# Kernel optimization log

Hardware: AMD Instinct MI355X
Metric: run time of the kernel (lower is better)

Reference implementation:

```python
import jax, jax.numpy as jnp
import numpy as np

FX, FY, CX, CY = 320.0, 320.0, 320.0, 240.0
N_MEAS, N_MP, N_KF = 2_000_000, 100_000, 2_000


def setup_inputs() -> dict:
    key = jax.random.key(0)
    k1, k2, k3, k4 = jax.random.split(key, 4)
    tMP = jax.random.normal(k1, (N_MP, 3), jnp.float32)
    # poses: near-identity with a +5 z-translation so projective depth stays away from 0
    tKF = jnp.eye(4, dtype=jnp.float32)[None] + 0.05 * jax.random.normal(k2, (N_KF, 4, 4), jnp.float32)
    tKF = tKF.at[:, 2, 3].add(5.0)
    idxMP = jnp.arange(N_MP, dtype=jnp.int32)
    idxKF = jnp.arange(N_KF, dtype=jnp.int32)
    mKF = jax.random.randint(k3, (N_MEAS,), 0, N_KF).astype(jnp.float32)
    mMP = jax.random.randint(k4, (N_MEAS,), 0, N_MP).astype(jnp.float32)
    measurements = jnp.stack([mKF, mMP], axis=1)  # [N, 2] float ids
    return {"measurements": measurements, "tMP": tMP, "tKF": tKF, "idxMP": idxMP, "idxKF": idxKF}


def reference(measurements, tMP, tKF, idxMP, idxKF):
    # ID -> row-index join. Original does an O(N*K)/O(N*M) broadcast equality via
    # torch.where; ids here are sorted unique, so a sorted join (searchsorted)
    # yields identical indices without materializing the N x M compare.
    iKF = jnp.searchsorted(idxKF, measurements[:, 0].astype(jnp.int32))
    iMP = jnp.searchsorted(idxMP, measurements[:, 1].astype(jnp.int32))
    # homogeneous map points: [M, 4]
    tMPhomo = jnp.concatenate([tMP, jnp.ones((tMP.shape[0], 1), tMP.dtype)], axis=1)
    # gather + batched 4x4 pose @ point: [N, 4]
    pts = jnp.einsum('nij,nj->ni', tKF[iKF], tMPhomo[iMP])
    # perspective divide + intrinsics scale
    ptx = pts[:, 0] / pts[:, 2] * FX + CX
    pty = pts[:, 1] / pts[:, 2] * FY + CY
    return jnp.stack([ptx, pty], axis=1)  # [N, 2]
```

## Files before the change

### kernel.cpp

```cpp
#include <hip/hip_runtime.h>
#include <hip/hip_bf16.h>

#define FXK 320.0f
#define FYK 320.0f
#define CXK 320.0f
#define CYK 240.0f

#define MAX_KF 2048

typedef float float4u __attribute__((ext_vector_type(4), aligned(4)));

__device__ __forceinline__ void unpack_mp(float4u q, bool sh,
                                          float& x, float& y, float& z) {
    x = sh ? q.y : q.x;
    y = sh ? q.z : q.y;
    z = sh ? q.w : q.z;
}

__device__ __forceinline__ float4 project2(const float4* __restrict__ sPose,
                                           int kfa, float xa, float ya, float za,
                                           int kfb, float xb, float yb, float zb) {
    const float4* Pa = sPose + kfa * 3;
    const float4* Pb = sPose + kfb * 3;
    float4 a0 = Pa[0], a1 = Pa[1], a2 = Pa[2];
    float4 b0 = Pb[0], b1 = Pb[1], b2 = Pb[2];
    float pxa = a0.x * xa + a0.y * ya + a0.z * za + a0.w;
    float pya = a1.x * xa + a1.y * ya + a1.z * za + a1.w;
    float pza = a2.x * xa + a2.y * ya + a2.z * za + a2.w;
    float pxb = b0.x * xb + b0.y * yb + b0.z * zb + b0.w;
    float pyb = b1.x * xb + b1.y * yb + b1.z * zb + b1.w;
    float pzb = b2.x * xb + b2.y * yb + b2.z * zb + b2.w;
    float ia = 1.0f / pza;
    float ib = 1.0f / pzb;
    float4 r;
    r.x = pxa * ia * FXK + CXK;
    r.y = pya * ia * FYK + CYK;
    r.z = pxb * ib * FXK + CXK;
    r.w = pyb * ib * FYK + CYK;
    return r;
}

__global__ __launch_bounds__(1024, 1) void proj_kernel(
    const float4* __restrict__ meas4,
    const float*  __restrict__ tMP,
    const float4* __restrict__ tKF4,
    float4*       __restrict__ out4,
    const float*  __restrict__ meas,
    float*        __restrict__ out,
    int n,
    int nKF,
    int nMPf)
{
    __shared__ float4 sPose[MAX_KF * 3];
    const int tid = threadIdx.x;
    const int nChunks = nKF * 3;
    for (int c = tid; c < nChunks; c += blockDim.x) {
        int pose = c / 3;
        int row  = c - pose * 3;
        sPose[c] = tKF4[pose * 4 + row];
    }
    __syncthreads();

    const int nPairs = n >> 1;
    const int bdim   = blockDim.x;
    const int tile   = bdim * 2;
    const int sweep  = gridDim.x * tile;
    const int last4  = nMPf - 4;

    for (int base = blockIdx.x * tile; base < nPairs; base += sweep) {
        int i0 = base + tid;
        int i1 = i0 + bdim;
        bool v0 = i0 < nPairs;
        bool v1 = i1 < nPairs;

        float4 m0 = meas4[v0 ? i0 : 0];
        float4 m1 = meas4[v1 ? i1 : 0];

        int kfA = (int)m0.x, mpA = (int)m0.y;
        int kfB = (int)m0.z, mpB = (int)m0.w;
        int kfC = (int)m1.x, mpC = (int)m1.y;
        int kfD = (int)m1.z, mpD = (int)m1.w;

        int oA = mpA * 3, oB = mpB * 3, oC = mpC * 3, oD = mpD * 3;
        int cA = oA > last4 ? last4 : oA;
        int cB = oB > last4 ? last4 : oB;
        int cC = oC > last4 ? last4 : oC;
        int cD = oD > last4 ? last4 : oD;
        float4u qA = *(const float4u*)(tMP + cA);
        float4u qB = *(const float4u*)(tMP + cB);
        float4u qC = *(const float4u*)(tMP + cC);
        float4u qD = *(const float4u*)(tMP + cD);

        float xA, yA, zA, xB, yB, zB, xC, yC, zC, xD, yD, zD;
        unpack_mp(qA, cA != oA, xA, yA, zA);
        unpack_mp(qB, cB != oB, xB, yB, zB);
        unpack_mp(qC, cC != oC, xC, yC, zC);
        unpack_mp(qD, cD != oD, xD, yD, zD);

        float4 r0 = project2(sPose, kfA, xA, yA, zA, kfB, xB, yB, zB);
        if (v0) out4[i0] = r0;
        float4 r1 = project2(sPose, kfC, xC, yC, zC, kfD, xD, yD, zD);
        if (v1) out4[i1] = r1;
    }

    if ((n & 1) && blockIdx.x == 0 && tid == 0) {
        int j = n - 1;
        int kf = (int)meas[2 * j + 0];
        int mp = (int)meas[2 * j + 1];
        float x = tMP[3 * mp + 0];
        float y = tMP[3 * mp + 1];
        float z = tMP[3 * mp + 2];
        const float4* P = sPose + kf * 3;
        float4 a0 = P[0], a1 = P[1], a2 = P[2];
        float px = a0.x * x + a0.y * y + a0.z * z + a0.w;
        float py = a1.x * x + a1.y * y + a1.z * z + a1.w;
        float pz = a2.x * x + a2.y * y + a2.z * z + a2.w;
        float inv = 1.0f / pz;
        out[2 * j + 0] = px * inv * FXK + CXK;
        out[2 * j + 1] = py * inv * FYK + CYK;
    }
}

extern "C" void kernel_launch(void* const* d_in, const int* in_sizes, int n_in,
                              void* d_out, int out_size, void* d_ws, size_t ws_size,
                              hipStream_t stream) {
    const float* meas = (const float*)d_in[0];
    const float* tMP  = (const float*)d_in[1];
    const float* tKF  = (const float*)d_in[2];

    int n    = in_sizes[0] / 2;
    int nMPf = in_sizes[1];
    int nKF  = in_sizes[2] / 16;
    if (nKF > MAX_KF) nKF = MAX_KF;

    int nPairs = n >> 1;
    int threads = 1024;
    int tile = threads * 2;
    int blocks = (nPairs + tile - 1) / tile;
    if (blocks > 256) blocks = 256;
    if (blocks < 1) blocks = 1;

    proj_kernel<<<blocks, threads, 0, stream>>>(
        (const float4*)meas, tMP, (const float4*)tKF,
        (float4*)d_out, meas, (float*)d_out, n, nKF, nMPf);
}
```

Measured before the change: 84.30 us.

## Repack map points to aligned float4, pad pose LDS stride, use nontemporal I/O

Adds a pre-pass kernel that copies the 3-float map points into a 16-byte aligned float4 workspace, so the main kernel gathers each point with one aligned load and no clamp or select logic. The shared pose table now uses a 13-float stride to spread LDS bank accesses for random keyframe lookups. Measurement loads and output stores become nontemporal to avoid polluting cache. The cost is an extra kernel launch and a copy of the map points into a 1.6MB workspace on every call, and the packed path only runs when the workspace is large enough.

After: 90.44 us. 1.07x slower.

```diff
diff --git a/kernel.cpp b/kernel.cpp
--- a/kernel.cpp
+++ b/kernel.cpp
@@ -1,5 +1,4 @@
 #include <hip/hip_runtime.h>
-#include <hip/hip_bf16.h>
 
 #define FXK 320.0f
 #define FYK 320.0f
@@ -7,8 +6,45 @@
 #define CYK 240.0f
 
 #define MAX_KF 2048
+#define PSTRIDE 13
 
+typedef float nf4 __attribute__((ext_vector_type(4)));
 typedef float float4u __attribute__((ext_vector_type(4), aligned(4)));
+
+__global__ void repack_mp_kernel(const float* __restrict__ tMP,
+                                 nf4* __restrict__ tMP4, int nMP) {
+    int i = blockIdx.x * blockDim.x + threadIdx.x;
+    int stride = gridDim.x * blockDim.x;
+    for (; i < nMP; i += stride) {
+        nf4 v;
+        v.x = tMP[3 * i + 0];
+        v.y = tMP[3 * i + 1];
+        v.z = tMP[3 * i + 2];
+        v.w = 0.0f;
+        tMP4[i] = v;
+    }
+}
+
+__device__ __forceinline__ nf4 project2(const float* __restrict__ sP,
+                                        int kfa, float xa, float ya, float za,
+                                        int kfb, float xb, float yb, float zb) {
+    const float* A = sP + kfa * PSTRIDE;
+    const float* B = sP + kfb * PSTRIDE;
+    float pxa = A[0] * xa + A[1] * ya + A[2]  * za + A[3];
+    float pya = A[4] * xa + A[5] * ya + A[6]  * za + A[7];
+    float pza = A[8] * xa + A[9] * ya + A[10] * za + A[11];
+    float pxb = B[0] * xb + B[1] * yb + B[2]  * zb + B[3];
+    float pyb = B[4] * xb + B[5] * yb + B[6]  * zb + B[7];
+    float pzb = B[8] * xb + B[9] * yb + B[10] * zb + B[11];
+    float ia = 1.0f / pza;
+    float ib = 1.0f / pzb;
+    nf4 r;
+    r.x = pxa * ia * FXK + CXK;
+    r.y = pya * ia * FYK + CYK;
+    r.z = pxb * ib * FXK + CXK;
+    r.w = pyb * ib * FYK + CYK;
+    return r;
+}
 
 __device__ __forceinline__ void unpack_mp(float4u q, bool sh,
                                           float& x, float& y, float& z) {
@@ -17,47 +53,28 @@
     z = sh ? q.w : q.z;
 }
 
-__device__ __forceinline__ float4 project2(const float4* __restrict__ sPose,
-                                           int kfa, float xa, float ya, float za,
-                                           int kfb, float xb, float yb, float zb) {
-    const float4* Pa = sPose + kfa * 3;
-    const float4* Pb = sPose + kfb * 3;
-    float4 a0 = Pa[0], a1 = Pa[1], a2 = Pa[2];
-    float4 b0 = Pb[0], b1 = Pb[1], b2 = Pb[2];
-    float pxa = a0.x * xa + a0.y * ya + a0.z * za + a0.w;
-    float pya = a1.x * xa + a1.y * ya + a1.z * za + a1.w;
-    float pza = a2.x * xa + a2.y * ya + a2.z * za + a2.w;
-    float pxb = b0.x * xb + b0.y * yb + b0.z * zb + b0.w;
-    float pyb = b1.x * xb + b1.y * yb + b1.z * zb + b1.w;
-    float pzb = b2.x * xb + b2.y * yb + b2.z * zb + b2.w;
-    float ia = 1.0f / pza;
-    float ib = 1.0f / pzb;
-    float4 r;
-    r.x = pxa * ia * FXK + CXK;
-    r.y = pya * ia * FYK + CYK;
-    r.z = pxb * ib * FXK + CXK;
-    r.w = pyb * ib * FYK + CYK;
-    return r;
-}
-
+template <bool PACKED>
 __global__ __launch_bounds__(1024, 1) void proj_kernel(
-    const float4* __restrict__ meas4,
+    const nf4*    __restrict__ meas4,
     const float*  __restrict__ tMP,
-    const float4* __restrict__ tKF4,
-    float4*       __restrict__ out4,
+    const nf4*    __restrict__ tMP4,
+    const nf4*    __restrict__ tKF4,
+    nf4*          __restrict__ out4,
     const float*  __restrict__ meas,
     float*        __restrict__ out,
     int n,
     int nKF,
     int nMPf)
 {
-    __shared__ float4 sPose[MAX_KF * 3];
+    __shared__ float sP[MAX_KF * PSTRIDE];
     const int tid = threadIdx.x;
     const int nChunks = nKF * 3;
     for (int c = tid; c < nChunks; c += blockDim.x) {
         int pose = c / 3;
         int row  = c - pose * 3;
-        sPose[c] = tKF4[pose * 4 + row];
+        nf4 v = tKF4[pose * 4 + row];
+        float* d = sP + pose * PSTRIDE + row * 4;
+        d[0] = v.x; d[1] = v.y; d[2] = v.z; d[3] = v.w;
     }
     __syncthreads();
 
@@ -73,34 +90,44 @@
         bool v0 = i0 < nPairs;
         bool v1 = i1 < nPairs;
 
-        float4 m0 = meas4[v0 ? i0 : 0];
-        float4 m1 = meas4[v1 ? i1 : 0];
+        nf4 m0 = __builtin_nontemporal_load(&meas4[v0 ? i0 : 0]);
+        nf4 m1 = __builtin_nontemporal_load(&meas4[v1 ? i1 : 0]);
 
         int kfA = (int)m0.x, mpA = (int)m0.y;
         int kfB = (int)m0.z, mpB = (int)m0.w;
         int kfC = (int)m1.x, mpC = (int)m1.y;
         int kfD = (int)m1.z, mpD = (int)m1.w;
 
-        int oA = mpA * 3, oB = mpB * 3, oC = mpC * 3, oD = mpD * 3;
-        int cA = oA > last4 ? last4 : oA;
-        int cB = oB > last4 ? last4 : oB;
-        int cC = oC > last4 ? last4 : oC;
-        int cD = oD > last4 ? last4 : oD;
-        float4u qA = *(const float4u*)(tMP + cA);
-        float4u qB = *(const float4u*)(tMP + cB);
-        float4u qC = *(const float4u*)(tMP + cC);
-        float4u qD = *(const float4u*)(tMP + cD);
+        float xA, yA, zA, xB, yB, zB, xC, yC, zC, xD, yD, zD;
+        if (PACKED) {
+            nf4 qA = tMP4[mpA];
+            nf4 qB = tMP4[mpB];
+            nf4 qC = tMP4[mpC];
+            nf4 qD = tMP4[mpD];
+            xA = qA.x; yA = qA.y; zA = qA.z;
+            xB = qB.x; yB = qB.y; zB = qB.z;
+            xC = qC.x; yC = qC.y; zC = qC.z;
+            xD = qD.x; yD = qD.y; zD = qD.z;
+        } else {
+            int oA = mpA * 3, oB = mpB * 3, oC = mpC * 3, oD = mpD * 3;
+            int cA = oA > last4 ? last4 : oA;
+            int cB = oB > last4 ? last4 : oB;
+            int cC = oC > last4 ? last4 : oC;
+            int cD = oD > last4 ? last4 : oD;
+            float4u qA = *(const float4u*)(tMP + cA);
+            float4u qB = *(const float4u*)(tMP + cB);
+            float4u qC = *(const float4u*)(tMP + cC);
+            float4u qD = *(const float4u*)(tMP + cD);
+            unpack_mp(qA, cA != oA, xA, yA, zA);
+            unpack_mp(qB, cB != oB, xB, yB, zB);
+            unpack_mp(qC, cC != oC, xC, yC, zC);
+            unpack_mp(qD, cD != oD, xD, yD, zD);
+        }
 
-        float xA, yA, zA, xB, yB, zB, xC, yC, zC, xD, yD, zD;
-        unpack_mp(qA, cA != oA, xA, yA, zA);
-        unpack_mp(qB, cB != oB, xB, yB, zB);
-        unpack_mp(qC, cC != oC, xC, yC, zC);
-        unpack_mp(qD, cD != oD, xD, yD, zD);
-
-        float4 r0 = project2(sPose, kfA, xA, yA, zA, kfB, xB, yB, zB);
-        if (v0) out4[i0] = r0;
-        float4 r1 = project2(sPose, kfC, xC, yC, zC, kfD, xD, yD, zD);
-        if (v1) out4[i1] = r1;
+        nf4 r0 = project2(sP, kfA, xA, yA, zA, kfB, xB, yB, zB);
+        if (v0) __builtin_nontemporal_store(r0, &out4[i0]);
+        nf4 r1 = project2(sP, kfC, xC, yC, zC, kfD, xD, yD, zD);
+        if (v1) __builtin_nontemporal_store(r1, &out4[i1]);
     }
 
     if ((n & 1) && blockIdx.x == 0 && tid == 0) {
@@ -110,11 +137,10 @@
         float x = tMP[3 * mp + 0];
         float y = tMP[3 * mp + 1];
         float z = tMP[3 * mp + 2];
-        const float4* P = sPose + kf * 3;
-        float4 a0 = P[0], a1 = P[1], a2 = P[2];
-        float px = a0.x * x + a0.y * y + a0.z * z + a0.w;
-        float py = a1.x * x + a1.y * y + a1.z * z + a1.w;
-        float pz = a2.x * x + a2.y * y + a2.z * z + a2.w;
+        const float* P = sP + kf * PSTRIDE;
+        float px = P[0] * x + P[1] * y + P[2]  * z + P[3];
+        float py = P[4] * x + P[5] * y + P[6]  * z + P[7];
+        float pz = P[8] * x + P[9] * y + P[10] * z + P[11];
         float inv = 1.0f / pz;
         out[2 * j + 0] = px * inv * FXK + CXK;
         out[2 * j + 1] = py * inv * FYK + CYK;
@@ -130,6 +156,7 @@
 
     int n    = in_sizes[0] / 2;
     int nMPf = in_sizes[1];
+    int nMP  = nMPf / 3;
     int nKF  = in_sizes[2] / 16;
     if (nKF > MAX_KF) nKF = MAX_KF;
 
@@ -140,7 +167,20 @@
     if (blocks > 256) blocks = 256;
     if (blocks < 1) blocks = 1;
 
-    proj_kernel<<<blocks, threads, 0, stream>>>(
-        (const float4*)meas, tMP, (const float4*)tKF,
-        (float4*)d_out, meas, (float*)d_out, n, nKF, nMPf);
+    bool packed = ws_size >= (size_t)nMP * sizeof(nf4);
+    if (packed) {
+        nf4* tMP4 = (nf4*)d_ws;
+        int rthreads = 256;
+        int rblocks = (nMP + rthreads - 1) / rthreads;
+        if (rblocks > 512) rblocks = 512;
+        if (rblocks < 1) rblocks = 1;
+        repack_mp_kernel<<<rblocks, rthreads, 0, stream>>>(tMP, tMP4, nMP);
+        proj_kernel<true><<<blocks, threads, 0, stream>>>(
+            (const nf4*)meas, tMP, tMP4, (const nf4*)tKF,
+            (nf4*)d_out, meas, (float*)d_out, n, nKF, nMPf);
+    } else {
+        proj_kernel<false><<<blocks, threads, 0, stream>>>(
+            (const nf4*)meas, tMP, (const nf4*)nullptr, (const nf4*)tKF,
+            (nf4*)d_out, meas, (float*)d_out, n, nKF, nMPf);
+    }
 }
```

## Drop shared-memory pose staging, gather poses from global with nontemporal streaming

Applied to the files above, without the earlier changes.

Removes the per-block copy of all keyframe poses into LDS and the barrier that follows, and reads pose rows straight from global memory, relying on L2/L1 caching of the small 128 KB pose table. Switches to 256-thread blocks with up to 2048 blocks, one measurement pair per thread, and nontemporal loads and stores for the streaming measurement and output data. This removes the LDS fill cost that 256 large blocks each paid and raises occupancy. In exchange, every pose access now goes through the cache hierarchy as a random gather instead of LDS.

Measured after the change: 100.1 us. +18.8%, slower.

```diff
diff --git a/kernel.cpp b/kernel.cpp
--- a/kernel.cpp
+++ b/kernel.cpp
@@ -1,120 +1,81 @@
 #include <hip/hip_runtime.h>
-#include <hip/hip_bf16.h>
 
 #define FXK 320.0f
 #define FYK 320.0f
 #define CXK 320.0f
 #define CYK 240.0f
 
-#define MAX_KF 2048
-
+typedef float nf4 __attribute__((ext_vector_type(4)));
 typedef float float4u __attribute__((ext_vector_type(4), aligned(4)));
 
-__device__ __forceinline__ void unpack_mp(float4u q, bool sh,
-                                          float& x, float& y, float& z) {
-    x = sh ? q.y : q.x;
-    y = sh ? q.z : q.y;
-    z = sh ? q.w : q.z;
-}
-
-__device__ __forceinline__ float4 project2(const float4* __restrict__ sPose,
-                                           int kfa, float xa, float ya, float za,
-                                           int kfb, float xb, float yb, float zb) {
-    const float4* Pa = sPose + kfa * 3;
-    const float4* Pb = sPose + kfb * 3;
-    float4 a0 = Pa[0], a1 = Pa[1], a2 = Pa[2];
-    float4 b0 = Pb[0], b1 = Pb[1], b2 = Pb[2];
-    float pxa = a0.x * xa + a0.y * ya + a0.z * za + a0.w;
-    float pya = a1.x * xa + a1.y * ya + a1.z * za + a1.w;
-    float pza = a2.x * xa + a2.y * ya + a2.z * za + a2.w;
-    float pxb = b0.x * xb + b0.y * yb + b0.z * zb + b0.w;
-    float pyb = b1.x * xb + b1.y * yb + b1.z * zb + b1.w;
-    float pzb = b2.x * xb + b2.y * yb + b2.z * zb + b2.w;
-    float ia = 1.0f / pza;
-    float ib = 1.0f / pzb;
-    float4 r;
-    r.x = pxa * ia * FXK + CXK;
-    r.y = pya * ia * FYK + CYK;
-    r.z = pxb * ib * FXK + CXK;
-    r.w = pyb * ib * FYK + CYK;
-    return r;
-}
-
-__global__ __launch_bounds__(1024, 1) void proj_kernel(
-    const float4* __restrict__ meas4,
+__global__ __launch_bounds__(256, 8) void proj_kernel(
+    const nf4*    __restrict__ meas4,
     const float*  __restrict__ tMP,
-    const float4* __restrict__ tKF4,
-    float4*       __restrict__ out4,
+    const nf4*    __restrict__ tKF4,
+    nf4*          __restrict__ out4,
     const float*  __restrict__ meas,
     float*        __restrict__ out,
     int n,
-    int nKF,
     int nMPf)
 {
-    __shared__ float4 sPose[MAX_KF * 3];
-    const int tid = threadIdx.x;
-    const int nChunks = nKF * 3;
-    for (int c = tid; c < nChunks; c += blockDim.x) {
-        int pose = c / 3;
-        int row  = c - pose * 3;
-        sPose[c] = tKF4[pose * 4 + row];
-    }
-    __syncthreads();
-
     const int nPairs = n >> 1;
-    const int bdim   = blockDim.x;
-    const int tile   = bdim * 2;
-    const int sweep  = gridDim.x * tile;
+    const int stride = gridDim.x * blockDim.x;
     const int last4  = nMPf - 4;
 
-    for (int base = blockIdx.x * tile; base < nPairs; base += sweep) {
-        int i0 = base + tid;
-        int i1 = i0 + bdim;
-        bool v0 = i0 < nPairs;
-        bool v1 = i1 < nPairs;
+    for (int i = blockIdx.x * blockDim.x + threadIdx.x; i < nPairs; i += stride) {
+        nf4 m = __builtin_nontemporal_load(&meas4[i]);
+        int kfA = (int)m.x, mpA = (int)m.y;
+        int kfB = (int)m.z, mpB = (int)m.w;
 
-        float4 m0 = meas4[v0 ? i0 : 0];
-        float4 m1 = meas4[v1 ? i1 : 0];
-
-        int kfA = (int)m0.x, mpA = (int)m0.y;
-        int kfB = (int)m0.z, mpB = (int)m0.w;
-        int kfC = (int)m1.x, mpC = (int)m1.y;
-        int kfD = (int)m1.z, mpD = (int)m1.w;
-
-        int oA = mpA * 3, oB = mpB * 3, oC = mpC * 3, oD = mpD * 3;
+        int oA = mpA * 3, oB = mpB * 3;
         int cA = oA > last4 ? last4 : oA;
         int cB = oB > last4 ? last4 : oB;
-        int cC = oC > last4 ? last4 : oC;
-        int cD = oD > last4 ? last4 : oD;
         float4u qA = *(const float4u*)(tMP + cA);
         float4u qB = *(const float4u*)(tMP + cB);
-        float4u qC = *(const float4u*)(tMP + cC);
-        float4u qD = *(const float4u*)(tMP + cD);
+        nf4 a0 = tKF4[kfA * 4 + 0];
+        nf4 a1 = tKF4[kfA * 4 + 1];
+        nf4 a2 = tKF4[kfA * 4 + 2];
+        nf4 b0 = tKF4[kfB * 4 + 0];
+        nf4 b1 = tKF4[kfB * 4 + 1];
+        nf4 b2 = tKF4[kfB * 4 + 2];
 
-        float xA, yA, zA, xB, yB, zB, xC, yC, zC, xD, yD, zD;
-        unpack_mp(qA, cA != oA, xA, yA, zA);
-        unpack_mp(qB, cB != oB, xB, yB, zB);
-        unpack_mp(qC, cC != oC, xC, yC, zC);
-        unpack_mp(qD, cD != oD, xD, yD, zD);
+        bool sA = cA != oA, sB = cB != oB;
+        float xA = sA ? qA.y : qA.x;
+        float yA = sA ? qA.z : qA.y;
+        float zA = sA ? qA.w : qA.z;
+        float xB = sB ? qB.y : qB.x;
+        float yB = sB ? qB.z : qB.y;
+        float zB = sB ? qB.w : qB.z;
 
-        float4 r0 = project2(sPose, kfA, xA, yA, zA, kfB, xB, yB, zB);
-        if (v0) out4[i0] = r0;
-        float4 r1 = project2(sPose, kfC, xC, yC, zC, kfD, xD, yD, zD);
-        if (v1) out4[i1] = r1;
+        float pxa = a0.x * xA + a0.y * yA + a0.z * zA + a0.w;
+        float pya = a1.x * xA + a1.y * yA + a1.z * zA + a1.w;
+        float pza = a2.x * xA + a2.y * yA + a2.z * zA + a2.w;
+        float pxb = b0.x * xB + b0.y * yB + b0.z * zB + b0.w;
+        float pyb = b1.x * xB + b1.y * yB + b1.z * zB + b1.w;
+        float pzb = b2.x * xB + b2.y * yB + b2.z * zB + b2.w;
+        float ia = 1.0f / pza;
+        float ib = 1.0f / pzb;
+        nf4 r;
+        r.x = pxa * ia * FXK + CXK;
+        r.y = pya * ia * FYK + CYK;
+        r.z = pxb * ib * FXK + CXK;
+        r.w = pyb * ib * FYK + CYK;
+        __builtin_nontemporal_store(r, &out4[i]);
     }
 
-    if ((n & 1) && blockIdx.x == 0 && tid == 0) {
+    if ((n & 1) && blockIdx.x == 0 && threadIdx.x == 0) {
         int j = n - 1;
         int kf = (int)meas[2 * j + 0];
         int mp = (int)meas[2 * j + 1];
         float x = tMP[3 * mp + 0];
         float y = tMP[3 * mp + 1];
         float z = tMP[3 * mp + 2];
-        const float4* P = sPose + kf * 3;
-        float4 a0 = P[0], a1 = P[1], a2 = P[2];
-        float px = a0.x * x + a0.y * y + a0.z * z + a0.w;
-        float py = a1.x * x + a1.y * y + a1.z * z + a1.w;
-        float pz = a2.x * x + a2.y * y + a2.z * z + a2.w;
+        nf4 p0 = tKF4[kf * 4 + 0];
+        nf4 p1 = tKF4[kf * 4 + 1];
+        nf4 p2 = tKF4[kf * 4 + 2];
+        float px = p0.x * x + p0.y * y + p0.z * z + p0.w;
+        float py = p1.x * x + p1.y * y + p1.z * z + p1.w;
+        float pz = p2.x * x + p2.y * y + p2.z * z + p2.w;
         float inv = 1.0f / pz;
         out[2 * j + 0] = px * inv * FXK + CXK;
         out[2 * j + 1] = py * inv * FYK + CYK;
@@ -130,17 +91,14 @@
 
     int n    = in_sizes[0] / 2;
     int nMPf = in_sizes[1];
-    int nKF  = in_sizes[2] / 16;
-    if (nKF > MAX_KF) nKF = MAX_KF;
 
     int nPairs = n >> 1;
-    int threads = 1024;
-    int tile = threads * 2;
-    int blocks = (nPairs + tile - 1) / tile;
-    if (blocks > 256) blocks = 256;
+    int threads = 256;
+    int blocks = (nPairs + threads - 1) / threads;
+    if (blocks > 2048) blocks = 2048;
     if (blocks < 1) blocks = 1;
 
     proj_kernel<<<blocks, threads, 0, stream>>>(
-        (const float4*)meas, tMP, (const float4*)tKF,
-        (float4*)d_out, meas, (float*)d_out, n, nKF, nMPf);
+        (const nf4*)meas, tMP, (const nf4*)tKF,
+        (nf4*)d_out, meas, (float*)d_out, n, nMPf);
 }
```
